# Kernel optimization log

Measured on AMD Instinct MI355X. Metric: run time of the kernel, lower is better.

The kernel has to match this reference:

```python
import jax, jax.numpy as jnp
import numpy as np

B, S, H, D = 8, 4096, 16, 128

def setup_inputs() -> dict:
    key = jax.random.key(0)
    kq, kk, kv = jax.random.split(key, 3)
    q = jax.random.normal(kq, (B, S, H, D), dtype=jnp.float32)
    k = jax.random.normal(kk, (B, S, H, D), dtype=jnp.float32)
    v = jax.random.normal(kv, (B, S, H, D), dtype=jnp.float32)
    return {"q": q, "k": k, "v": v}

def reference(q, k, v):
    # Efficient (linear) attention: softmax K over sequence, softmax Q over feature dim,
    # then context = K^T V per (batch, head), out = Q @ context. Vectorized over heads.
    k_sm = jax.nn.softmax(k, axis=1)          # softmax over S  (B,S,H,D)
    q_sm = jax.nn.softmax(q, axis=-1)         # softmax over D  (B,S,H,D)
    context = jnp.einsum('bshd,bshe->bhde', k_sm, v)   # (B,H,Dk,Dv)
    out = jnp.einsum('bshd,bhde->bshe', q_sm, context) # (B,S,H,Dv)
    return out
```

## Files before the change

### kernel.cpp

```cpp
#include <hip/hip_runtime.h>

using bf16x8 = __attribute__((ext_vector_type(8))) short;
using f32x4  = __attribute__((ext_vector_type(4))) float;

static constexpr int NB = 8;
static constexpr int NS = 4096;
static constexpr int NH = 16;
static constexpr int ND = 128;
static constexpr int BH = NB * NH;
static constexpr int HD = NH * ND;

__device__ inline unsigned pack2(float a, float b) {
    unsigned ua = __float_as_uint(a), ub = __float_as_uint(b);
    ua += 0x7fffu + ((ua >> 16) & 1u);
    ub += 0x7fffu + ((ub >> 16) & 1u);
    return (ua >> 16) | (ub & 0xffff0000u);
}

__device__ inline int swz2(int row) { return (row ^ (row >> 2)) & 3; }

template <int NC>
__global__ __launch_bounds__(256, 3)
void ctx_mfma(const float* __restrict__ kk, const float* __restrict__ vv,
              float* __restrict__ pctx_t, float* __restrict__ pden) {
    constexpr int SC = NS / NC;
    constexpr int T  = SC / 32;
    __shared__ __align__(16) unsigned short aL[2][128][32];
    __shared__ __align__(16) unsigned short bL[2][128][32];

    const int blk = blockIdx.x, bh = blk / NC, c = blk % NC;
    const int b = bh >> 4, h = bh & 15;
    const int tid = threadIdx.x, lane = tid & 63, wv = tid >> 6;
    const int r15 = lane & 15, hi = lane >> 4;
    const size_t base = (size_t)b * NS * HD + (size_t)h * ND;

    const int d0 = (tid & 31) * 4;
    const int sg = tid >> 5;

    float dsum[4] = {0.f, 0.f, 0.f, 0.f};

    auto issue = [&](int t, float4* kq, float4* vq) {
        const size_t s0 = (size_t)(c * SC + t * 32 + 4 * sg);
        const float* kp = kk + base + s0 * HD + d0;
        const float* vp = vv + base + s0 * HD + d0;
#pragma unroll
        for (int j = 0; j < 4; ++j) kq[j] = *(const float4*)(kp + (size_t)j * HD);
#pragma unroll
        for (int j = 0; j < 4; ++j) vq[j] = *(const float4*)(vp + (size_t)j * HD);
    };

    f32x4 acc[4][4];
#pragma unroll
    for (int m = 0; m < 4; ++m)
#pragma unroll
        for (int n = 0; n < 4; ++n) acc[m][n] = (f32x4){0.f, 0.f, 0.f, 0.f};

    const int wd = wv >> 1, we = wv & 1;

    auto mma = [&](int buf) {
        bf16x8 af[4], bfv[4];
#pragma unroll
        for (int m = 0; m < 4; ++m) {
            const int row = 64 * wd + 16 * m + r15;
            const int pc0 = (2 * hi) ^ (swz2(row) << 1);
            af[m] = *(const bf16x8*)&aL[buf][row][pc0 * 4];
        }
#pragma unroll
        for (int n = 0; n < 4; ++n) {
            const int row = 64 * we + 16 * n + r15;
            const int pc0 = (2 * hi) ^ (swz2(row) << 1);
            bfv[n] = *(const bf16x8*)&bL[buf][row][pc0 * 4];
        }
#pragma unroll
        for (int m = 0; m < 4; ++m)
#pragma unroll
            for (int n = 0; n < 4; ++n)
                acc[m][n] = __builtin_amdgcn_mfma_f32_16x16x32_bf16(
                    af[m], bfv[n], acc[m][n], 0, 0, 0);
    };

    float4 kq[4], vq[4];
    issue(0, kq, vq);

    for (int t = 0; t < T; ++t) {
        const float* kf = (const float*)kq;
        const float* vf = (const float*)vq;
        uint2 pa[4], pb[4];
#pragma unroll
        for (int i = 0; i < 4; ++i) {
            float e0 = __expf(kf[0 + i]), e1 = __expf(kf[4 + i]);
            float e2 = __expf(kf[8 + i]), e3 = __expf(kf[12 + i]);
            dsum[i] += (e0 + e1) + (e2 + e3);
            pa[i] = make_uint2(pack2(e0, e1), pack2(e2, e3));
            pb[i] = make_uint2(pack2(vf[0 + i], vf[4 + i]),
                               pack2(vf[8 + i], vf[12 + i]));
        }
        if (t + 1 < T) issue(t + 1, kq, vq);
        const int buf = t & 1;
#pragma unroll
        for (int i = 0; i < 4; ++i) {
            const int row = d0 + i;
            const int slot = sg ^ (swz2(row) << 1);
            *(uint2*)&aL[buf][row][slot * 4] = pa[i];
            *(uint2*)&bL[buf][row][slot * 4] = pb[i];
        }
        __syncthreads();
        mma(buf);
    }

    __syncthreads();
    float* dr = (float*)&aL[0][0][0];
    *(float4*)&dr[sg * 128 + d0] = make_float4(dsum[0], dsum[1], dsum[2], dsum[3]);
    __syncthreads();
    if (tid < 128) {
        float s = 0.f;
#pragma unroll
        for (int r = 0; r < 8; ++r) s += dr[r * 128 + tid];
        pden[(size_t)blk * 128 + tid] = s;
    }

    float* po = pctx_t + (size_t)blk * (ND * ND);
#pragma unroll
    for (int m = 0; m < 4; ++m)
#pragma unroll
        for (int n = 0; n < 4; ++n) {
            const int e  = 64 * we + 16 * n + r15;
            const int dd = 64 * wd + 16 * m + 4 * hi;
            *(f32x4*)&po[e * ND + dd] = acc[m][n];
        }
}

__global__ void ctx_combine(const float* __restrict__ pctx_t,
                            const float* __restrict__ pden,
                            unsigned short* __restrict__ ctx_t, int nc) {
    const int gid = blockIdx.x * 256 + threadIdx.x;
    const size_t w = (size_t)gid * 2;
    const int bh = (int)(w >> 14);
    const int wi = (int)(w & 16383);
    const int dd = wi & 127;
    float s0 = 0.f, s1 = 0.f, dn0 = 0.f, dn1 = 0.f;
    for (int c2 = 0; c2 < nc; ++c2) {
        const float* p  = pctx_t + (((size_t)(bh * nc + c2)) << 14) + wi;
        const float* pd = pden + (size_t)(bh * nc + c2) * ND + dd;
        s0 += p[0]; s1 += p[1];
        dn0 += pd[0]; dn1 += pd[1];
    }
    *(unsigned*)&ctx_t[w] = pack2(s0 / dn0, s1 / dn1);
}

__global__ __launch_bounds__(256, 2)
void out_mfma(const float* __restrict__ qq,
              const unsigned short* __restrict__ ctx_t,
              float* __restrict__ out) {
    __shared__ __align__(16) unsigned short cL[128][128];
    __shared__ __align__(16) unsigned short qL[2][32][128];
    __shared__ float qd[2][32];

    const int blk = blockIdx.x, bh = blk >> 3, c = blk & 7;
    const int b = bh >> 4, h = bh & 15;
    const int tid = threadIdx.x, lane = tid & 63, wv = tid >> 6;
    const int r15 = lane & 15, hi = lane >> 4;

    {
        const unsigned short* src = ctx_t + ((size_t)bh << 14);
#pragma unroll
        for (int j = 0; j < 8; ++j) {
            const int g = tid + 256 * j;
            const int e = g >> 4, cs = g & 15;
            uint4 t4 = *(const uint4*)&src[e * 128 + cs * 8];
            *(uint4*)&cL[e][(cs ^ (e & 15)) * 8] = t4;
        }
    }

    const size_t qbase = (size_t)b * NS * HD + (size_t)h * ND;
    const int s_blk = c * 512;

    auto stageq = [&](int t, int buf) {
#pragma unroll
        for (int jj = 0; jj < 2; ++jj) {
            const int g = tid + 256 * jj;
            const int s = g >> 4, cs = g & 15;
            const float* qp = qq + qbase + (size_t)(s_blk + t * 32 + s) * HD + cs * 8;
            float x[8];
            *(float4*)&x[0] = *(const float4*)qp;
            *(float4*)&x[4] = *(const float4*)(qp + 4);
            float ps = 0.f;
            unsigned pw[4];
#pragma unroll
            for (int j2 = 0; j2 < 4; ++j2) {
                float e0 = __expf(x[2 * j2]), e1 = __expf(x[2 * j2 + 1]);
                ps += e0 + e1;
                pw[j2] = pack2(e0, e1);
            }
            ps += __shfl_xor(ps, 1);
            ps += __shfl_xor(ps, 2);
            ps += __shfl_xor(ps, 4);
            ps += __shfl_xor(ps, 8);
            *(uint4*)&qL[buf][s][(cs ^ (s & 15)) * 8] =
                make_uint4(pw[0], pw[1], pw[2], pw[3]);
            if ((lane & 15) == 0) qd[buf][s] = ps;
        }
    };

    __syncthreads();

    bf16x8 bfr[2][4];
#pragma unroll
    for (int n = 0; n < 2; ++n) {
        const int e = 32 * wv + 16 * n + r15;
#pragma unroll
        for (int ks = 0; ks < 4; ++ks) {
            const int cw = (4 * ks + hi) ^ (e & 15);
            bfr[n][ks] = *(const bf16x8*)&cL[e][cw * 8];
        }
    }

    stageq(0, 0);
    for (int t = 0; t < 16; ++t) {
        __syncthreads();
        if (t + 1 < 16) stageq(t + 1, (t + 1) & 1);
        const int buf = t & 1;

        f32x4 acc[2][2];
#pragma unroll
        for (int m = 0; m < 2; ++m)
#pragma unroll
            for (int n = 0; n < 2; ++n) acc[m][n] = (f32x4){0.f, 0.f, 0.f, 0.f};

#pragma unroll
        for (int ks = 0; ks < 4; ++ks) {
            bf16x8 af[2];
#pragma unroll
            for (int m = 0; m < 2; ++m) {
                const int s = 16 * m + r15;
                const int cw = (4 * ks + hi) ^ (s & 15);
                af[m] = *(const bf16x8*)&qL[buf][s][cw * 8];
            }
#pragma unroll
            for (int m = 0; m < 2; ++m)
#pragma unroll
                for (int n = 0; n < 2; ++n)
                    acc[m][n] = __builtin_amdgcn_mfma_f32_16x16x32_bf16(
                        af[m], bfr[n][ks], acc[m][n], 0, 0, 0);
        }

#pragma unroll
        for (int m = 0; m < 2; ++m) {
            const int sl0 = 16 * m + 4 * hi;
            const float i0 = 1.f / qd[buf][sl0];
            const float i1 = 1.f / qd[buf][sl0 + 1];
            const float i2 = 1.f / qd[buf][sl0 + 2];
            const float i3 = 1.f / qd[buf][sl0 + 3];
            const int srow = s_blk + t * 32 + sl0;
            float* ob = out + ((size_t)b * NS + srow) * HD + (size_t)h * ND;
#pragma unroll
            for (int n = 0; n < 2; ++n) {
                const int e = 32 * wv + 16 * n + r15;
                ob[0 * HD + e] = acc[m][n][0] * i0;
                ob[1 * HD + e] = acc[m][n][1] * i1;
                ob[2 * HD + e] = acc[m][n][2] * i2;
                ob[3 * HD + e] = acc[m][n][3] * i3;
            }
        }
    }
}

extern "C" void kernel_launch(void* const* d_in, const int* in_sizes, int n_in,
                              void* d_out, int out_size, void* d_ws, size_t ws_size,
                              hipStream_t stream) {
    (void)in_sizes; (void)n_in; (void)out_size;
    const float* q = (const float*)d_in[0];
    const float* k = (const float*)d_in[1];
    const float* v = (const float*)d_in[2];
    float* out = (float*)d_out;

    auto need = [](size_t nc) -> size_t {
        return 4ull * ((size_t)BH * nc * ND * ND + (size_t)BH * nc * ND) +
               2ull * (size_t)BH * ND * ND;
    };
    const int nc = (ws_size >= need(8)) ? 8
                 : (ws_size >= need(4)) ? 4
                 : (ws_size >= need(2)) ? 2 : 1;

    float* pctx_t = (float*)d_ws;
    float* pden   = pctx_t + (size_t)BH * nc * ND * ND;
    unsigned short* ctx_t = (unsigned short*)(pden + (size_t)BH * nc * ND);

    if (nc == 8)
        ctx_mfma<8><<<BH * 8, 256, 0, stream>>>(k, v, pctx_t, pden);
    else if (nc == 4)
        ctx_mfma<4><<<BH * 4, 256, 0, stream>>>(k, v, pctx_t, pden);
    else if (nc == 2)
        ctx_mfma<2><<<BH * 2, 256, 0, stream>>>(k, v, pctx_t, pden);
    else
        ctx_mfma<1><<<BH * 1, 256, 0, stream>>>(k, v, pctx_t, pden);

    ctx_combine<<<(BH * ND * ND / 2) / 256, 256, 0, stream>>>(pctx_t, pden, ctx_t, nc);

    out_mfma<<<BH * 8, 256, 0, stream>>>(q, ctx_t, out);
}
```

Before: 265.9 us.

## Restructure context kernel into 1024-thread blocks covering head pairs with specialized K/V waves

The context kernel now runs 1024-thread blocks, each covering two adjacent heads. Eight waves load and exponentiate K while the other eight load and pack V, so the heads' 256 contiguous floats are read as full rows. The main loop is unrolled by two with ping-pong register buffers, the LDS swizzle widens to 3 bits, and the sequence split drops from 8 chunks to 4. This aims to improve global coalescing and reduce partial-context traffic and combine work, but it lowers the number of blocks and puts more threads on each barrier.

```diff
diff --git a/kernel.cpp b/kernel.cpp
--- a/kernel.cpp
+++ b/kernel.cpp
@@ -17,115 +17,135 @@
     return (ua >> 16) | (ub & 0xffff0000u);
 }
 
-__device__ inline int swz2(int row) { return (row ^ (row >> 2)) & 3; }
+__device__ inline int swz3(int row) { return (row ^ (row >> 2)) & 7; }
 
 template <int NC>
-__global__ __launch_bounds__(256, 3)
+__global__ __launch_bounds__(1024, 4)
 void ctx_mfma(const float* __restrict__ kk, const float* __restrict__ vv,
               float* __restrict__ pctx_t, float* __restrict__ pden) {
     constexpr int SC = NS / NC;
     constexpr int T  = SC / 32;
-    __shared__ __align__(16) unsigned short aL[2][128][32];
-    __shared__ __align__(16) unsigned short bL[2][128][32];
-
-    const int blk = blockIdx.x, bh = blk / NC, c = blk % NC;
-    const int b = bh >> 4, h = bh & 15;
-    const int tid = threadIdx.x, lane = tid & 63, wv = tid >> 6;
-    const int r15 = lane & 15, hi = lane >> 4;
-    const size_t base = (size_t)b * NS * HD + (size_t)h * ND;
-
-    const int d0 = (tid & 31) * 4;
-    const int sg = tid >> 5;
+    __shared__ __align__(16) unsigned short aL[2][2][128][32];
+    __shared__ __align__(16) unsigned short bL[2][2][128][32];
+
+    const int blk = blockIdx.x, bhp = blk / NC, c = blk % NC;
+    const int b = bhp >> 3, hp = bhp & 7;
+    const int tid = threadIdx.x, l = tid & 63, wv = tid >> 6;
+    const int r15 = l & 15, hi = l >> 4;
+
+    const size_t base = (size_t)b * NS * HD + (size_t)hp * 256;
+
+    const bool isK = (wv < 8);
+    const int  wk  = isK ? wv : (wv - 8);
+    const float* src = isK ? kk : vv;
+    const int hl = l >> 5;
+    const int d0 = (l & 31) << 2;
 
     float dsum[4] = {0.f, 0.f, 0.f, 0.f};
 
-    auto issue = [&](int t, float4* kq, float4* vq) {
-        const size_t s0 = (size_t)(c * SC + t * 32 + 4 * sg);
-        const float* kp = kk + base + s0 * HD + d0;
-        const float* vp = vv + base + s0 * HD + d0;
-#pragma unroll
-        for (int j = 0; j < 4; ++j) kq[j] = *(const float4*)(kp + (size_t)j * HD);
-#pragma unroll
-        for (int j = 0; j < 4; ++j) vq[j] = *(const float4*)(vp + (size_t)j * HD);
-    };
-
-    f32x4 acc[4][4];
-#pragma unroll
-    for (int m = 0; m < 4; ++m)
+    auto issue = [&](int t, float4* q) {
+        const size_t s0 = (size_t)(c * SC + t * 32 + 4 * wk);
+        const float* p = src + base + s0 * HD + (size_t)l * 4;
+#pragma unroll
+        for (int j = 0; j < 4; ++j) q[j] = *(const float4*)(p + (size_t)j * HD);
+    };
+
+    auto pack_store = [&](int buf, const float4* q) {
+        const float* f = (const float*)q;
+        if (isK) {
+#pragma unroll
+            for (int i = 0; i < 4; ++i) {
+                float e0 = __expf(f[0 + i]), e1 = __expf(f[4 + i]);
+                float e2 = __expf(f[8 + i]), e3 = __expf(f[12 + i]);
+                dsum[i] += (e0 + e1) + (e2 + e3);
+                const int row = d0 + i;
+                const int slot = wk ^ swz3(row);
+                *(uint2*)&aL[buf][hl][row][slot * 4] =
+                    make_uint2(pack2(e0, e1), pack2(e2, e3));
+            }
+        } else {
+#pragma unroll
+            for (int i = 0; i < 4; ++i) {
+                const int row = d0 + i;
+                const int slot = wk ^ swz3(row);
+                *(uint2*)&bL[buf][hl][row][slot * 4] =
+                    make_uint2(pack2(f[0 + i], f[4 + i]),
+                               pack2(f[8 + i], f[12 + i]));
+            }
+        }
+    };
+
+    const int hm = wv >> 3, sub = wv & 7, wd = sub >> 1, we = sub & 1;
+
+    f32x4 acc[2][4];
+#pragma unroll
+    for (int m = 0; m < 2; ++m)
 #pragma unroll
         for (int n = 0; n < 4; ++n) acc[m][n] = (f32x4){0.f, 0.f, 0.f, 0.f};
 
-    const int wd = wv >> 1, we = wv & 1;
-
     auto mma = [&](int buf) {
-        bf16x8 af[4], bfv[4];
-#pragma unroll
-        for (int m = 0; m < 4; ++m) {
-            const int row = 64 * wd + 16 * m + r15;
-            const int pc0 = (2 * hi) ^ (swz2(row) << 1);
-            af[m] = *(const bf16x8*)&aL[buf][row][pc0 * 4];
+        bf16x8 af[2], bf[4];
+#pragma unroll
+        for (int m = 0; m < 2; ++m) {
+            const int row = 32 * wd + 16 * m + r15;
+            const int v = swz3(row);
+            uint2 r0 = *(const uint2*)&aL[buf][hm][row][((2 * hi) ^ v) * 4];
+            uint2 r1 = *(const uint2*)&aL[buf][hm][row][((2 * hi + 1) ^ v) * 4];
+            uint4 u = make_uint4(r0.x, r0.y, r1.x, r1.y);
+            af[m] = __builtin_bit_cast(bf16x8, u);
         }
 #pragma unroll
         for (int n = 0; n < 4; ++n) {
             const int row = 64 * we + 16 * n + r15;
-            const int pc0 = (2 * hi) ^ (swz2(row) << 1);
-            bfv[n] = *(const bf16x8*)&bL[buf][row][pc0 * 4];
-        }
-#pragma unroll
-        for (int m = 0; m < 4; ++m)
+            const int v = swz3(row);
+            uint2 r0 = *(const uint2*)&bL[buf][hm][row][((2 * hi) ^ v) * 4];
+            uint2 r1 = *(const uint2*)&bL[buf][hm][row][((2 * hi + 1) ^ v) * 4];
+            uint4 u = make_uint4(r0.x, r0.y, r1.x, r1.y);
+            bf[n] = __builtin_bit_cast(bf16x8, u);
+        }
+#pragma unroll
+        for (int m = 0; m < 2; ++m)
 #pragma unroll
             for (int n = 0; n < 4; ++n)
                 acc[m][n] = __builtin_amdgcn_mfma_f32_16x16x32_bf16(
-                    af[m], bfv[n], acc[m][n], 0, 0, 0);
-    };
-
-    float4 kq[4], vq[4];
-    issue(0, kq, vq);
-
-    for (int t = 0; t < T; ++t) {
-        const float* kf = (const float*)kq;
-        const float* vf = (const float*)vq;
-        uint2 pa[4], pb[4];
-#pragma unroll
-        for (int i = 0; i < 4; ++i) {
-            float e0 = __expf(kf[0 + i]), e1 = __expf(kf[4 + i]);
-            float e2 = __expf(kf[8 + i]), e3 = __expf(kf[12 + i]);
-            dsum[i] += (e0 + e1) + (e2 + e3);
-            pa[i] = make_uint2(pack2(e0, e1), pack2(e2, e3));
-            pb[i] = make_uint2(pack2(vf[0 + i], vf[4 + i]),
-                               pack2(vf[8 + i], vf[12 + i]));
-        }
-        if (t + 1 < T) issue(t + 1, kq, vq);
-        const int buf = t & 1;
-#pragma unroll
-        for (int i = 0; i < 4; ++i) {
-            const int row = d0 + i;
-            const int slot = sg ^ (swz2(row) << 1);
-            *(uint2*)&aL[buf][row][slot * 4] = pa[i];
-            *(uint2*)&bL[buf][row][slot * 4] = pb[i];
-        }
+                    af[m], bf[n], acc[m][n], 0, 0, 0);
+    };
+
+    float4 qa[4], qb[4];
+    issue(0, qa);
+    for (int t = 0; t < T; t += 2) {
+        if (t + 1 < T) issue(t + 1, qb);
+        pack_store(t & 1, qa);
         __syncthreads();
-        mma(buf);
+        mma(t & 1);
+        if (t + 2 < T) issue(t + 2, qa);
+        pack_store((t + 1) & 1, qb);
+        __syncthreads();
+        mma((t + 1) & 1);
     }
 
     __syncthreads();
-    float* dr = (float*)&aL[0][0][0];
-    *(float4*)&dr[sg * 128 + d0] = make_float4(dsum[0], dsum[1], dsum[2], dsum[3]);
+    float* dr = (float*)&aL[0][0][0][0];
+    if (isK)
+        *(float4*)&dr[(hl * 8 + wk) * 128 + d0] =
+            make_float4(dsum[0], dsum[1], dsum[2], dsum[3]);
     __syncthreads();
-    if (tid < 128) {
+    if (tid < 256) {
+        const int head = tid >> 7, d = tid & 127;
         float s = 0.f;
 #pragma unroll
-        for (int r = 0; r < 8; ++r) s += dr[r * 128 + tid];
-        pden[(size_t)blk * 128 + tid] = s;
-    }
-
-    float* po = pctx_t + (size_t)blk * (ND * ND);
-#pragma unroll
-    for (int m = 0; m < 4; ++m)
+        for (int w = 0; w < 8; ++w) s += dr[(head * 8 + w) * 128 + d];
+        const int bh_g = b * 16 + hp * 2 + head;
+        pden[((size_t)bh_g * NC + c) * ND + d] = s;
+    }
+
+    float* po = pctx_t + (((size_t)(b * 16 + hp * 2 + hm) * NC + c) << 14);
+#pragma unroll
+    for (int m = 0; m < 2; ++m)
 #pragma unroll
         for (int n = 0; n < 4; ++n) {
             const int e  = 64 * we + 16 * n + r15;
-            const int dd = 64 * wd + 16 * m + 4 * hi;
+            const int dd = 32 * wd + 16 * m + 4 * hi;
             *(f32x4*)&po[e * ND + dd] = acc[m][n];
         }
 }
@@ -278,22 +298,18 @@
         return 4ull * ((size_t)BH * nc * ND * ND + (size_t)BH * nc * ND) +
                2ull * (size_t)BH * ND * ND;
     };
-    const int nc = (ws_size >= need(8)) ? 8
-                 : (ws_size >= need(4)) ? 4
-                 : (ws_size >= need(2)) ? 2 : 1;
+    const int nc = (ws_size >= need(4)) ? 4 : (ws_size >= need(2)) ? 2 : 1;
 
     float* pctx_t = (float*)d_ws;
     float* pden   = pctx_t + (size_t)BH * nc * ND * ND;
     unsigned short* ctx_t = (unsigned short*)(pden + (size_t)BH * nc * ND);
 
-    if (nc == 8)
-        ctx_mfma<8><<<BH * 8, 256, 0, stream>>>(k, v, pctx_t, pden);
-    else if (nc == 4)
-        ctx_mfma<4><<<BH * 4, 256, 0, stream>>>(k, v, pctx_t, pden);
+    if (nc == 4)
+        ctx_mfma<4><<<64 * 4, 1024, 0, stream>>>(k, v, pctx_t, pden);
     else if (nc == 2)
-        ctx_mfma<2><<<BH * 2, 256, 0, stream>>>(k, v, pctx_t, pden);
+        ctx_mfma<2><<<64 * 2, 1024, 0, stream>>>(k, v, pctx_t, pden);
     else
-        ctx_mfma<1><<<BH * 1, 256, 0, stream>>>(k, v, pctx_t, pden);
+        ctx_mfma<1><<<64 * 1, 1024, 0, stream>>>(k, v, pctx_t, pden);
 
     ctx_combine<<<(BH * ND * ND / 2) / 256, 256, 0, stream>>>(pctx_t, pden, ctx_t, nc);
 
```

Measured after the change: 248.1 us. -6.7%, faster.

## Load K/V head pairs via global_load_lds DMA with separate LDS transform stage

Applied to the files above, without the earlier changes.

The context kernel now has each 512-thread block handle two adjacent heads. Each warp copies contiguous 1KB rows of K and V straight into LDS with global_load_lds, instead of loading float4 into registers. A separate transform pass reads the raw fp32 tile from LDS, applies exp and the denominator sum, packs to bf16 into an MFMA-friendly image, and runs MFMA every second 16-row tile. The goal is wider, fully coalesced global reads and less register pressure, at the cost of an extra LDS round trip and two barriers per tile.

```diff
diff --git a/kernel.cpp b/kernel.cpp
--- a/kernel.cpp
+++ b/kernel.cpp
@@ -17,37 +17,59 @@
     return (ua >> 16) | (ub & 0xffff0000u);
 }
 
-__device__ inline int swz2(int row) { return (row ^ (row >> 2)) & 3; }
-
 template <int NC>
-__global__ __launch_bounds__(256, 3)
+__global__ __launch_bounds__(512, 4)
 void ctx_mfma(const float* __restrict__ kk, const float* __restrict__ vv,
               float* __restrict__ pctx_t, float* __restrict__ pden) {
     constexpr int SC = NS / NC;
-    constexpr int T  = SC / 32;
-    __shared__ __align__(16) unsigned short aL[2][128][32];
-    __shared__ __align__(16) unsigned short bL[2][128][32];
-
-    const int blk = blockIdx.x, bh = blk / NC, c = blk % NC;
-    const int b = bh >> 4, h = bh & 15;
-    const int tid = threadIdx.x, lane = tid & 63, wv = tid >> 6;
-    const int r15 = lane & 15, hi = lane >> 4;
-    const size_t base = (size_t)b * NS * HD + (size_t)h * ND;
-
-    const int d0 = (tid & 31) * 4;
-    const int sg = tid >> 5;
-
-    float dsum[4] = {0.f, 0.f, 0.f, 0.f};
-
-    auto issue = [&](int t, float4* kq, float4* vq) {
-        const size_t s0 = (size_t)(c * SC + t * 32 + 4 * sg);
-        const float* kp = kk + base + s0 * HD + d0;
-        const float* vp = vv + base + s0 * HD + d0;
-#pragma unroll
-        for (int j = 0; j < 4; ++j) kq[j] = *(const float4*)(kp + (size_t)j * HD);
-#pragma unroll
-        for (int j = 0; j < 4; ++j) vq[j] = *(const float4*)(vp + (size_t)j * HD);
-    };
+    constexpr int T  = SC / 16;
+    __shared__ __align__(16) float raw[2][16][256];
+    __shared__ __align__(16) unsigned short img[2][2][4][2][128][4];
+
+    const int blk = blockIdx.x, bhp = blk / NC, c = blk % NC;
+    const int b = bhp >> 3, hp = bhp & 7;
+    const int tid = threadIdx.x, l = tid & 63, wv = tid >> 6;
+    const int r15 = l & 15, hi = l >> 4;
+
+    const size_t gbase = (size_t)b * NS * HD + (size_t)hp * 256;
+
+    auto dma_tile = [&](int t) {
+        const int s0 = c * SC + t * 16;
+#pragma unroll
+        for (int j = 0; j < 4; ++j) {
+            const int ch = wv * 4 + j;
+            const int arr = ch >> 4, s_i = ch & 15;
+            const float* g = (arr ? vv : kk) + gbase + (size_t)(s0 + s_i) * HD + l * 4;
+            __builtin_amdgcn_global_load_lds(
+                (const __attribute__((address_space(1))) void*)g,
+                (__attribute__((address_space(3))) void*)&raw[arr][s_i][0],
+                16, 0, 0);
+        }
+    };
+
+    const int arr_t = tid >> 8;
+    const int dcol  = tid & 255;
+    const int hl_t = dcol >> 7, d_t = dcol & 127;
+    float dsum = 0.f;
+
+    auto transform = [&](int buf) {
+        float x[16];
+#pragma unroll
+        for (int s = 0; s < 16; ++s) x[s] = raw[arr_t][s][dcol];
+        if (arr_t == 0) {
+#pragma unroll
+            for (int s = 0; s < 16; ++s) { x[s] = __expf(x[s]); dsum += x[s]; }
+        }
+#pragma unroll
+        for (int t4 = 0; t4 < 4; ++t4)
+            *(uint2*)&img[buf][arr_t][t4][hl_t][d_t][0] =
+                make_uint2(pack2(x[4 * t4], x[4 * t4 + 1]),
+                           pack2(x[4 * t4 + 2], x[4 * t4 + 3]));
+    };
+
+    const int hm = wv >> 2, sub = wv & 3, wd = sub >> 1, we = sub & 1;
+    const int ibuf = hi >> 1;
+    const int t4a = (2 * hi) & 3, t4b = (2 * hi + 1) & 3;
 
     f32x4 acc[4][4];
 #pragma unroll
@@ -55,21 +77,23 @@
 #pragma unroll
         for (int n = 0; n < 4; ++n) acc[m][n] = (f32x4){0.f, 0.f, 0.f, 0.f};
 
-    const int wd = wv >> 1, we = wv & 1;
-
-    auto mma = [&](int buf) {
+    auto mma_pair = [&]() {
         bf16x8 af[4], bfv[4];
 #pragma unroll
         for (int m = 0; m < 4; ++m) {
             const int row = 64 * wd + 16 * m + r15;
-            const int pc0 = (2 * hi) ^ (swz2(row) << 1);
-            af[m] = *(const bf16x8*)&aL[buf][row][pc0 * 4];
+            uint2 lo = *(const uint2*)&img[ibuf][0][t4a][hm][row][0];
+            uint2 h2 = *(const uint2*)&img[ibuf][0][t4b][hm][row][0];
+            uint4 u = make_uint4(lo.x, lo.y, h2.x, h2.y);
+            af[m] = __builtin_bit_cast(bf16x8, u);
         }
 #pragma unroll
         for (int n = 0; n < 4; ++n) {
             const int row = 64 * we + 16 * n + r15;
-            const int pc0 = (2 * hi) ^ (swz2(row) << 1);
-            bfv[n] = *(const bf16x8*)&bL[buf][row][pc0 * 4];
+            uint2 lo = *(const uint2*)&img[ibuf][1][t4a][hm][row][0];
+            uint2 h2 = *(const uint2*)&img[ibuf][1][t4b][hm][row][0];
+            uint4 u = make_uint4(lo.x, lo.y, h2.x, h2.y);
+            bfv[n] = __builtin_bit_cast(bf16x8, u);
         }
 #pragma unroll
         for (int m = 0; m < 4; ++m)
@@ -79,47 +103,22 @@
                     af[m], bfv[n], acc[m][n], 0, 0, 0);
     };
 
-    float4 kq[4], vq[4];
-    issue(0, kq, vq);
-
+    dma_tile(0);
     for (int t = 0; t < T; ++t) {
-        const float* kf = (const float*)kq;
-        const float* vf = (const float*)vq;
-        uint2 pa[4], pb[4];
-#pragma unroll
-        for (int i = 0; i < 4; ++i) {
-            float e0 = __expf(kf[0 + i]), e1 = __expf(kf[4 + i]);
-            float e2 = __expf(kf[8 + i]), e3 = __expf(kf[12 + i]);
-            dsum[i] += (e0 + e1) + (e2 + e3);
-            pa[i] = make_uint2(pack2(e0, e1), pack2(e2, e3));
-            pb[i] = make_uint2(pack2(vf[0 + i], vf[4 + i]),
-                               pack2(vf[8 + i], vf[12 + i]));
-        }
-        if (t + 1 < T) issue(t + 1, kq, vq);
-        const int buf = t & 1;
-#pragma unroll
-        for (int i = 0; i < 4; ++i) {
-            const int row = d0 + i;
-            const int slot = sg ^ (swz2(row) << 1);
-            *(uint2*)&aL[buf][row][slot * 4] = pa[i];
-            *(uint2*)&bL[buf][row][slot * 4] = pb[i];
-        }
         __syncthreads();
-        mma(buf);
+        transform(t & 1);
+        __syncthreads();
+        if (t + 1 < T) dma_tile(t + 1);
+        if (t & 1) mma_pair();
     }
 
     __syncthreads();
-    float* dr = (float*)&aL[0][0][0];
-    *(float4*)&dr[sg * 128 + d0] = make_float4(dsum[0], dsum[1], dsum[2], dsum[3]);
-    __syncthreads();
-    if (tid < 128) {
-        float s = 0.f;
-#pragma unroll
-        for (int r = 0; r < 8; ++r) s += dr[r * 128 + tid];
-        pden[(size_t)blk * 128 + tid] = s;
-    }
-
-    float* po = pctx_t + (size_t)blk * (ND * ND);
+    if (tid < 256) {
+        const int bh_g = b * 16 + hp * 2 + hl_t;
+        pden[((size_t)bh_g * NC + c) * ND + d_t] = dsum;
+    }
+
+    float* po = pctx_t + (((size_t)(b * 16 + hp * 2 + hm) * NC + c) << 14);
 #pragma unroll
     for (int m = 0; m < 4; ++m)
 #pragma unroll
@@ -287,13 +286,13 @@
     unsigned short* ctx_t = (unsigned short*)(pden + (size_t)BH * nc * ND);
 
     if (nc == 8)
-        ctx_mfma<8><<<BH * 8, 256, 0, stream>>>(k, v, pctx_t, pden);
+        ctx_mfma<8><<<64 * 8, 512, 0, stream>>>(k, v, pctx_t, pden);
     else if (nc == 4)
-        ctx_mfma<4><<<BH * 4, 256, 0, stream>>>(k, v, pctx_t, pden);
+        ctx_mfma<4><<<64 * 4, 512, 0, stream>>>(k, v, pctx_t, pden);
     else if (nc == 2)
-        ctx_mfma<2><<<BH * 2, 256, 0, stream>>>(k, v, pctx_t, pden);
+        ctx_mfma<2><<<64 * 2, 512, 0, stream>>>(k, v, pctx_t, pden);
     else
-        ctx_mfma<1><<<BH * 1, 256, 0, stream>>>(k, v, pctx_t, pden);
+        ctx_mfma<1><<<64 * 1, 512, 0, stream>>>(k, v, pctx_t, pden);
 
     ctx_combine<<<(BH * ND * ND / 2) / 256, 256, 0, stream>>>(pctx_t, pden, ctx_t, nc);
 
```

Result: faster. 259.8 us (-2.3%).
